# Optimization experiments

Measured on AMD Instinct MI355X. Metric: run time of the kernel, lower is better.

Reference implementation:

```python
import jax, jax.numpy as jnp
import numpy as np
from jax import lax

EPS_LN = 1e-5
EPS_BN = 1e-5

def layernorm(x, g, b):
    m = x.mean(-1, keepdims=True)
    v = x.var(-1, keepdims=True)
    return (x - m) / jnp.sqrt(v + EPS_LN) * g + b

def conv(x, w, b):
    y = lax.conv_general_dilated(x, w, (1, 1), 'SAME', dimension_numbers=('NCHW', 'OIHW', 'NCHW'))
    return y + b[None, :, None, None]

def bnorm(x, g, b, m, v):
    # BatchNorm2d in eval mode (running stats)
    return (x - m[None, :, None, None]) / jnp.sqrt(v[None, :, None, None] + EPS_BN) * g[None, :, None, None] + b[None, :, None, None]

def maxpool2(x):
    return lax.reduce_window(x, -jnp.inf, lax.max, (1, 1, 2, 2), (1, 1, 2, 2), 'VALID')

def l2norm_rows(x):
    n = jnp.linalg.norm(x, axis=1, keepdims=True)
    return x / jnp.maximum(n, 1e-12)

def fastslow(x, sw, sb, fw, fb, lng, lnb, lr, decay):
    # one hebbian fast-weight update step (torch does this in no_grad on x.detach())
    xs = lax.stop_gradient(x)
    fw = fw * decay
    fb = fb * decay
    slow_out = xs @ sw.T + sb
    xn = l2norm_rows(xs)
    son = l2norm_rows(slow_out)
    hebb = son.T @ xn / xs.shape[0]          # [out,in] outer-product update
    fw = fw + lr * hebb
    wn = jnp.linalg.norm(fw, axis=1, keepdims=True)
    fw = jnp.where(wn > 0.25, fw * (0.25 / (wn + 1e-8)), fw)
    fb = jnp.clip(fb + lr * son.mean(0), -0.2, 0.2)
    fw = lax.stop_gradient(fw)
    fb = lax.stop_gradient(fb)
    out = x @ (sw + fw).T + (sb + fb)
    return layernorm(out, lng, lnb)

def forward(x, c1_w, c1_b, bn1_g, bn1_b, bn1_m, bn1_v,
            c2_w, c2_b, bn2_g, bn2_b, bn2_m, bn2_v,
            c3_w, c3_b, bn3_g, bn3_b, bn3_m, bn3_v,
            core_w, core_b, core_lng, core_lnb,
            fp_sw, fp_sb, fp_fw, fp_fb, fp_lng, fp_lnb,
            sp_sw, sp_sb, sp_fw, sp_fb, sp_lng, sp_lnb,
            int_w, int_b, int_lng, int_lnb, mem,
            cn_w1, cn_b1, cn_lng, cn_lnb, cn_w2, cn_b2,
            pr_w, pr_b, pr_lng, pr_lnb, cl_w, cl_b):
    # encoder (dropout layers are identity in eval)
    h = jax.nn.relu(bnorm(conv(x, c1_w, c1_b), bn1_g, bn1_b, bn1_m, bn1_v)); h = maxpool2(h)
    h = jax.nn.relu(bnorm(conv(h, c2_w, c2_b), bn2_g, bn2_b, bn2_m, bn2_v)); h = maxpool2(h)
    h = jax.nn.relu(bnorm(conv(h, c3_w, c3_b), bn3_g, bn3_b, bn3_m, bn3_v))
    h = h.mean((2, 3))  # AdaptiveAvgPool2d((1,1)) + Flatten -> [B,256]
    # core
    hc = jax.nn.relu(layernorm(h @ core_w.T + core_b, core_lng, core_lnb))
    # dual system: memory EMA (no_grad), fast/slow hebbian paths, integrator
    mem_new = lax.stop_gradient(0.9 * mem + 0.1 * hc.mean(0, keepdims=True))
    fast_out = fastslow(hc, fp_sw, fp_sb, fp_fw, fp_fb, fp_lng, fp_lnb, 0.015, 0.95)
    slow_out = fastslow(hc + 0.3 * mem_new, sp_sw, sp_sb, sp_fw, sp_fb, sp_lng, sp_lnb, 0.005, 0.97)
    comb = jnp.concatenate([fast_out, slow_out], axis=1)
    hd = layernorm(comb @ int_w.T + int_b, int_lng, int_lnb)
    hd = hd + hc  # residual
    # consciousness: phi from eigen-entropy of feature covariance (no_grad)
    a = lax.stop_gradient(hd)
    am = a.mean(0, keepdims=True)
    ast = jnp.std(a, axis=0, keepdims=True, ddof=1) + 1e-6
    an = (a - am) / ast
    n = a.shape[0]
    cov = an.T @ an / (n - 1) + 1e-4 * jnp.eye(a.shape[1], dtype=a.dtype)
    eigs = jnp.clip(jnp.linalg.eigvalsh(cov), 0.0, None)
    en = eigs / (eigs.sum() + 1e-8)
    entropy = -(en * jnp.log(en + 1e-8)).sum()
    phi = entropy / jnp.log(jnp.asarray(float(a.shape[1]), a.dtype))
    phi_eff = jnp.clip(0.3 * phi, 0.0, 1.0)  # running_phi starts at 0: 0.7*0 + 0.3*phi
    net = jax.nn.relu(layernorm(hd @ cn_w1.T + cn_b1, cn_lng, cn_lnb)) @ cn_w2.T + cn_b2
    strength = jax.nn.sigmoid((phi_eff - 0.1) * 5.0)
    coef = jnp.where(phi_eff > 0.1, strength, 0.1)
    hcon = hd + coef * net
    # projection + classifier
    hp = jax.nn.relu(layernorm(hcon @ pr_w.T + pr_b, pr_lng, pr_lnb))
    return hp @ cl_w.T + cl_b

def setup_inputs() -> dict:
    key = jax.random.key(0)
    ks = iter(jax.random.split(key, 64))
    def nrm(shape, s=0.05):
        return jax.random.normal(next(ks), shape, jnp.float32) * s
    B, D = 512, 256
    d = {}
    d['x'] = jax.random.normal(next(ks), (B, 3, 32, 32), jnp.float32)
    for i, (co, ci) in enumerate([(64, 3), (128, 64), (256, 128)], 1):
        d[f'c{i}_w'] = nrm((co, ci, 3, 3))
        d[f'c{i}_b'] = jnp.zeros((co,), jnp.float32)
        d[f'bn{i}_g'] = jnp.ones((co,), jnp.float32)
        d[f'bn{i}_b'] = jnp.zeros((co,), jnp.float32)
        d[f'bn{i}_m'] = jnp.zeros((co,), jnp.float32)
        d[f'bn{i}_v'] = jnp.ones((co,), jnp.float32)
    d['core_w'] = nrm((D, D)); d['core_b'] = jnp.zeros((D,), jnp.float32)
    d['core_lng'] = jnp.ones((D,), jnp.float32); d['core_lnb'] = jnp.zeros((D,), jnp.float32)
    for p in ['fp', 'sp']:
        d[f'{p}_sw'] = nrm((D, D)); d[f'{p}_sb'] = jnp.zeros((D,), jnp.float32)
        d[f'{p}_fw'] = nrm((D, D), 0.01); d[f'{p}_fb'] = jnp.zeros((D,), jnp.float32)
        d[f'{p}_lng'] = jnp.ones((D,), jnp.float32); d[f'{p}_lnb'] = jnp.zeros((D,), jnp.float32)
    d['int_w'] = nrm((D, 2 * D)); d['int_b'] = jnp.zeros((D,), jnp.float32)
    d['int_lng'] = jnp.ones((D,), jnp.float32); d['int_lnb'] = jnp.zeros((D,), jnp.float32)
    d['mem'] = jnp.zeros((1, D), jnp.float32)
    d['cn_w1'] = nrm((D, D)); d['cn_b1'] = jnp.zeros((D,), jnp.float32)
    d['cn_lng'] = jnp.ones((D,), jnp.float32); d['cn_lnb'] = jnp.zeros((D,), jnp.float32)
    d['cn_w2'] = nrm((D, D)); d['cn_b2'] = jnp.zeros((D,), jnp.float32)
    d['pr_w'] = nrm((128, D)); d['pr_b'] = jnp.zeros((128,), jnp.float32)
    d['pr_lng'] = jnp.ones((128,), jnp.float32); d['pr_lnb'] = jnp.zeros((128,), jnp.float32)
    d['cl_w'] = nrm((10, 128)); d['cl_b'] = jnp.zeros((10,), jnp.float32)
    return d

def reference(x, c1_w, c1_b, bn1_g, bn1_b, bn1_m, bn1_v,
              c2_w, c2_b, bn2_g, bn2_b, bn2_m, bn2_v,
              c3_w, c3_b, bn3_g, bn3_b, bn3_m, bn3_v,
              core_w, core_b, core_lng, core_lnb,
              fp_sw, fp_sb, fp_fw, fp_fb, fp_lng, fp_lnb,
              sp_sw, sp_sb, sp_fw, sp_fb, sp_lng, sp_lnb,
              int_w, int_b, int_lng, int_lnb, mem,
              cn_w1, cn_b1, cn_lng, cn_lnb, cn_w2, cn_b2,
              pr_w, pr_b, pr_lng, pr_lnb, cl_w, cl_b):
    return forward(x, c1_w, c1_b, bn1_g, bn1_b, bn1_m, bn1_v,
                   c2_w, c2_b, bn2_g, bn2_b, bn2_m, bn2_v,
                   c3_w, c3_b, bn3_g, bn3_b, bn3_m, bn3_v,
                   core_w, core_b, core_lng, core_lnb,
                   fp_sw, fp_sb, fp_fw, fp_fb, fp_lng, fp_lnb,
                   sp_sw, sp_sb, sp_fw, sp_fb, sp_lng, sp_lnb,
                   int_w, int_b, int_lng, int_lnb, mem,
                   cn_w1, cn_b1, cn_lng, cn_lnb, cn_w2, cn_b2,
                   pr_w, pr_b, pr_lng, pr_lnb, cl_w, cl_b)
```

## Files before the change

kernel.cpp:

```cpp
#include <hip/hip_runtime.h>
#include <hip/hip_bf16.h>

template<int NT>
__device__ __forceinline__ float block_sum(float v, float* red, int t) {
  red[t] = v; __syncthreads();
#pragma unroll
  for (int s = NT/2; s > 0; s >>= 1) {
    if (t < s) red[t] += red[t+s];
    __syncthreads();
  }
  float r = red[0];
  __syncthreads();
  return r;
}

template<int DIN>
__device__ __forceinline__ float dot_f32_row(const float* __restrict__ wr, const float* __restrict__ xs) {
  float acc = 0.f;
  const float4* wp = reinterpret_cast<const float4*>(wr);
#pragma unroll 4
  for (int i = 0; i < DIN/4; ++i) {
    float4 w4 = wp[i];
    acc += w4.x*xs[i*4] + w4.y*xs[i*4+1] + w4.z*xs[i*4+2] + w4.w*xs[i*4+3];
  }
  return acc;
}

__global__ __launch_bounds__(256) void k_conv1(const float* __restrict__ x, const float* __restrict__ w1,
    const float* __restrict__ cb, const float* __restrict__ g, const float* __restrict__ bb,
    const float* __restrict__ m, const float* __restrict__ v, float* __restrict__ p1)
{
  __shared__ float xs[3][34][34];
  __shared__ float ws1[64*27];
  __shared__ float A1[64], B1[64];
  int b = blockIdx.x, t = threadIdx.x;
  float* xsf = &xs[0][0][0];
  for (int i = t; i < 3*34*34; i += 256) xsf[i] = 0.f;
  for (int i = t; i < 64*27; i += 256) ws1[i] = w1[i];
  if (t < 64) {
    float sc = g[t] * rsqrtf(v[t] + 1e-5f);
    A1[t] = sc;
    B1[t] = (cb[t] - m[t])*sc + bb[t];
  }
  __syncthreads();
  for (int i = t; i < 3*1024; i += 256) {
    int ci = i >> 10, rem = i & 1023, y = rem >> 5, xx = rem & 31;
    xs[ci][y+1][xx+1] = x[((size_t)b*3 + ci)*1024 + rem];
  }
  __syncthreads();
  int py = t >> 4, px = t & 15;
  int y0 = py*2, x0 = px*2;
  for (int co = 0; co < 64; ++co) {
    float a00=0.f,a01=0.f,a10=0.f,a11=0.f;
#pragma unroll
    for (int ci = 0; ci < 3; ++ci) {
      const float* xb = &xs[ci][y0][x0];
      float r0a=xb[0],r0b=xb[1],r0c=xb[2],r0d=xb[3];
      float r1a=xb[34],r1b=xb[35],r1c=xb[36],r1d=xb[37];
      float r2a=xb[68],r2b=xb[69],r2c=xb[70],r2d=xb[71];
      float r3a=xb[102],r3b=xb[103],r3c=xb[104],r3d=xb[105];
      const float* wp = &ws1[co*27 + ci*9];
      float ww0=wp[0],ww1=wp[1],ww2=wp[2],ww3=wp[3],ww4=wp[4],ww5=wp[5],ww6=wp[6],ww7=wp[7],ww8=wp[8];
      a00 += ww0*r0a+ww1*r0b+ww2*r0c + ww3*r1a+ww4*r1b+ww5*r1c + ww6*r2a+ww7*r2b+ww8*r2c;
      a01 += ww0*r0b+ww1*r0c+ww2*r0d + ww3*r1b+ww4*r1c+ww5*r1d + ww6*r2b+ww7*r2c+ww8*r2d;
      a10 += ww0*r1a+ww1*r1b+ww2*r1c + ww3*r2a+ww4*r2b+ww5*r2c + ww6*r3a+ww7*r3b+ww8*r3c;
      a11 += ww0*r1b+ww1*r1c+ww2*r1d + ww3*r2b+ww4*r2c+ww5*r2d + ww6*r3b+ww7*r3c+ww8*r3d;
    }
    float sc = A1[co], sh = B1[co];
    float vmax = fmaxf(fmaxf(a00*sc+sh, a01*sc+sh), fmaxf(a10*sc+sh, a11*sc+sh));
    vmax = fmaxf(vmax, 0.f);
    p1[(((size_t)b*64 + co)*16 + py)*16 + px] = vmax;
  }
}

__global__ __launch_bounds__(256) void k_conv2(const float* __restrict__ p1, const float* __restrict__ w2,
    const float* __restrict__ cb, const float* __restrict__ g, const float* __restrict__ bb,
    const float* __restrict__ m, const float* __restrict__ v, float* __restrict__ p2)
{
  __shared__ float xs[64][18][18];
  __shared__ float wchT[576*5];
  __shared__ float A2[128], B2[128];
  int b = blockIdx.x, t = threadIdx.x;
  float* xsf = &xs[0][0][0];
  for (int i = t; i < 64*18*18; i += 256) xsf[i] = 0.f;
  if (t < 128) {
    float sc = g[t] * rsqrtf(v[t] + 1e-5f);
    A2[t] = sc;
    B2[t] = (cb[t] - m[t])*sc + bb[t];
  }
  __syncthreads();
  for (int i = t; i < 64*256; i += 256) {
    int ci = i >> 8, rem = i & 255, y = rem >> 4, xx = rem & 15;
    xs[ci][y+1][xx+1] = p1[((size_t)b*64 + ci)*256 + rem];
  }
  int lane = t & 3, pos = t >> 2;
  int py = pos >> 3, px = pos & 7;
  int y0 = py*2, x0 = px*2;
  for (int it = 0; it < 32; ++it) {
    __syncthreads();
    for (int i = t; i < 2304; i += 256) {
      int rem = i % 576, co = i / 576;
      wchT[rem*5 + co] = w2[(size_t)it*2304 + i];
    }
    __syncthreads();
    float a00=0.f,a01=0.f,a10=0.f,a11=0.f;
    for (int ci = 0; ci < 64; ++ci) {
      const float* xb = &xs[ci][y0][x0];
      float r0a=xb[0],r0b=xb[1],r0c=xb[2],r0d=xb[3];
      float r1a=xb[18],r1b=xb[19],r1c=xb[20],r1d=xb[21];
      float r2a=xb[36],r2b=xb[37],r2c=xb[38],r2d=xb[39];
      float r3a=xb[54],r3b=xb[55],r3c=xb[56],r3d=xb[57];
      const float* wp = &wchT[(ci*9)*5 + lane];
      float ww0=wp[0],ww1=wp[5],ww2=wp[10],ww3=wp[15],ww4=wp[20],ww5=wp[25],ww6=wp[30],ww7=wp[35],ww8=wp[40];
      a00 += ww0*r0a+ww1*r0b+ww2*r0c + ww3*r1a+ww4*r1b+ww5*r1c + ww6*r2a+ww7*r2b+ww8*r2c;
      a01 += ww0*r0b+ww1*r0c+ww2*r0d + ww3*r1b+ww4*r1c+ww5*r1d + ww6*r2b+ww7*r2c+ww8*r2d;
      a10 += ww0*r1a+ww1*r1b+ww2*r1c + ww3*r2a+ww4*r2b+ww5*r2c + ww6*r3a+ww7*r3b+ww8*r3c;
      a11 += ww0*r1b+ww1*r1c+ww2*r1d + ww3*r2b+ww4*r2c+ww5*r2d + ww6*r3b+ww7*r3c+ww8*r3d;
    }
    int co = it*4 + lane;
    float sc = A2[co], sh = B2[co];
    float vmax = fmaxf(fmaxf(a00*sc+sh, a01*sc+sh), fmaxf(a10*sc+sh, a11*sc+sh));
    vmax = fmaxf(vmax, 0.f);
    p2[(((size_t)b*128 + co)*8 + py)*8 + px] = vmax;
  }
}

__global__ __launch_bounds__(256) void k_conv3(const float* __restrict__ p2, const float* __restrict__ w3,
    const float* __restrict__ cb, const float* __restrict__ g, const float* __restrict__ bb,
    const float* __restrict__ m, const float* __restrict__ v, float* __restrict__ h)
{
  __shared__ float xs[128][10][10];
  __shared__ float wchT[1152*17];
  __shared__ float A3[256], B3[256];
  __shared__ float red2[256];
  int b = blockIdx.x, t = threadIdx.x;
  float* xsf = &xs[0][0][0];
  for (int i = t; i < 128*100; i += 256) xsf[i] = 0.f;
  {
    float sc = g[t] * rsqrtf(v[t] + 1e-5f);
    A3[t] = sc;
    B3[t] = (cb[t] - m[t])*sc + bb[t];
  }
  __syncthreads();
  for (int i = t; i < 128*64; i += 256) {
    int ci = i >> 6, rem = i & 63, y = rem >> 3, xx = rem & 7;
    xs[ci][y+1][xx+1] = p2[((size_t)b*128 + ci)*64 + rem];
  }
  int lane = t & 15, cluster = t >> 4;
  int cy = cluster >> 2, cx = cluster & 3;
  int y0 = cy*2, x0 = cx*2;
  for (int it = 0; it < 16; ++it) {
    __syncthreads();
    for (int i = t; i < 18432; i += 256) {
      int rem = i % 1152, co = i / 1152;
      wchT[rem*17 + co] = w3[(size_t)it*18432 + i];
    }
    __syncthreads();
    float a00=0.f,a01=0.f,a10=0.f,a11=0.f;
    for (int ci = 0; ci < 128; ++ci) {
      const float* xb = &xs[ci][y0][x0];
      float r0a=xb[0],r0b=xb[1],r0c=xb[2],r0d=xb[3];
      float r1a=xb[10],r1b=xb[11],r1c=xb[12],r1d=xb[13];
      float r2a=xb[20],r2b=xb[21],r2c=xb[22],r2d=xb[23];
      float r3a=xb[30],r3b=xb[31],r3c=xb[32],r3d=xb[33];
      const float* wp = &wchT[(ci*9)*17 + lane];
      float ww0=wp[0],ww1=wp[17],ww2=wp[34],ww3=wp[51],ww4=wp[68],ww5=wp[85],ww6=wp[102],ww7=wp[119],ww8=wp[136];
      a00 += ww0*r0a+ww1*r0b+ww2*r0c + ww3*r1a+ww4*r1b+ww5*r1c + ww6*r2a+ww7*r2b+ww8*r2c;
      a01 += ww0*r0b+ww1*r0c+ww2*r0d + ww3*r1b+ww4*r1c+ww5*r1d + ww6*r2b+ww7*r2c+ww8*r2d;
      a10 += ww0*r1a+ww1*r1b+ww2*r1c + ww3*r2a+ww4*r2b+ww5*r2c + ww6*r3a+ww7*r3b+ww8*r3c;
      a11 += ww0*r1b+ww1*r1c+ww2*r1d + ww3*r2b+ww4*r2c+ww5*r2d + ww6*r3b+ww7*r3c+ww8*r3d;
    }
    int co = it*16 + lane;
    float sc = A3[co], sh = B3[co];
    float local = fmaxf(a00*sc+sh,0.f)+fmaxf(a01*sc+sh,0.f)+fmaxf(a10*sc+sh,0.f)+fmaxf(a11*sc+sh,0.f);
    red2[cluster*16 + lane] = local;
    __syncthreads();
    if (t < 16) {
      float s2 = 0.f;
      for (int c2 = 0; c2 < 16; ++c2) s2 += red2[c2*16 + t];
      h[(size_t)b*256 + it*16 + t] = s2 * (1.f/64.f);
    }
  }
}

template<int DIN, int DOUT, bool RELU, bool RESID>
__global__ __launch_bounds__(DOUT) void k_lin_ln(
    const float* __restrict__ in, const float* __restrict__ W, const float* __restrict__ bias,
    const float* __restrict__ g, const float* __restrict__ be,
    const float* __restrict__ resid, float* __restrict__ out, int ostride, int ooff)
{
  __shared__ float xs[DIN];
  __shared__ float red[DOUT];
  int b = blockIdx.x, t = threadIdx.x;
  for (int i = t; i < DIN; i += DOUT) xs[i] = in[(size_t)b*DIN + i];
  __syncthreads();
  float acc = dot_f32_row<DIN>(W + (size_t)t*DIN, xs) + bias[t];
  float mean = block_sum<DOUT>(acc, red, t) * (1.f/DOUT);
  float dv = acc - mean;
  float var = block_sum<DOUT>(dv*dv, red, t) * (1.f/DOUT);
  float y = dv * rsqrtf(var + 1e-5f) * g[t] + be[t];
  if (RELU) y = fmaxf(y, 0.f);
  if (RESID) y += resid[(size_t)b*DOUT + t];
  out[(size_t)b*ostride + ooff + t] = y;
}

__global__ __launch_bounds__(256) void k_lin_rownorm(const float* __restrict__ in, const float* __restrict__ sw,
    const float* __restrict__ sb, float* __restrict__ sout, float* __restrict__ xninv, float* __restrict__ sninv)
{
  int b = blockIdx.x, t = threadIdx.x;
  __shared__ float xs[256];
  __shared__ float red[256];
  xs[t] = in[(size_t)b*256 + t];
  __syncthreads();
  float acc = dot_f32_row<256>(sw + (size_t)t*256, xs) + sb[t];
  sout[(size_t)b*256 + t] = acc;
  float xn2 = block_sum<256>(xs[t]*xs[t], red, t);
  float sn2 = block_sum<256>(acc*acc, red, t);
  if (t == 0) {
    xninv[b] = 1.f / fmaxf(sqrtf(xn2), 1e-12f);
    sninv[b] = 1.f / fmaxf(sqrtf(sn2), 1e-12f);
  }
}

__global__ __launch_bounds__(256) void k_hebb(const float* __restrict__ x, const float* __restrict__ s,
    const float* __restrict__ xninv, const float* __restrict__ sninv,
    const float* __restrict__ sw, const float* __restrict__ fw,
    const float* __restrict__ sb, const float* __restrict__ fb,
    float lr, float decay, float* __restrict__ weff, float* __restrict__ beff)
{
  int o = blockIdx.x, t = threadIdx.x;
  __shared__ float c[512];
  __shared__ float sonb[512];
  __shared__ float red[256];
  for (int b = t; b < 512; b += 256) {
    float son = s[(size_t)b*256 + o] * sninv[b];
    sonb[b] = son;
    c[b] = son * xninv[b];
  }
  __syncthreads();
  float acc = 0.f;
  for (int b = 0; b < 512; ++b) acc += c[b] * x[(size_t)b*256 + t];
  float hebb = acc * (1.f/512.f);
  float fwn = fw[(size_t)o*256 + t] * decay + lr * hebb;
  float wn2 = block_sum<256>(fwn*fwn, red, t);
  float wn = sqrtf(wn2);
  float scale = (wn > 0.25f) ? 0.25f/(wn + 1e-8f) : 1.f;
  weff[(size_t)o*256 + t] = sw[(size_t)o*256 + t] + fwn*scale;
  float sm = block_sum<256>(sonb[t] + sonb[t+256], red, t) * (1.f/512.f);
  if (t == 0) {
    float fbe = fb[o] * decay + lr * sm;
    fbe = fminf(fmaxf(fbe, -0.2f), 0.2f);
    beff[o] = sb[o] + fbe;
  }
}

__global__ __launch_bounds__(256) void k_mem(const float* __restrict__ hc, const float* __restrict__ mem,
                                             float* __restrict__ memnew)
{
  int t = threadIdx.x;
  float s = 0.f;
  for (int b = 0; b < 512; ++b) s += hc[(size_t)b*256 + t];
  memnew[t] = 0.9f*mem[t] + 0.1f*(s * (1.f/512.f));
}

__global__ __launch_bounds__(256) void k_x2(const float* __restrict__ hc, const float* __restrict__ memnew,
                                            float* __restrict__ x2)
{
  int i = blockIdx.x*256 + threadIdx.x;
  x2[i] = hc[i] + 0.3f*memnew[i & 255];
}

__global__ __launch_bounds__(256) void k_colstats(const float* __restrict__ hd, float* __restrict__ am,
                                                  float* __restrict__ ainv)
{
  int t = threadIdx.x;
  float s1 = 0.f;
  for (int b = 0; b < 512; ++b) s1 += hd[(size_t)b*256 + t];
  float mean = s1 * (1.f/512.f);
  float s2 = 0.f;
  for (int b = 0; b < 512; ++b) { float dv = hd[(size_t)b*256 + t] - mean; s2 += dv*dv; }
  am[t] = mean;
  ainv[t] = 1.f/(sqrtf(s2 * (1.f/511.f)) + 1e-6f);
}

__global__ __launch_bounds__(256) void k_cov(const float* __restrict__ hd, const float* __restrict__ am,
    const float* __restrict__ ainv, float* __restrict__ cov)
{
  int i = blockIdx.x, t = threadIdx.x;
  __shared__ float ci[512];
  float ami = am[i], aii = ainv[i];
  for (int b = t; b < 512; b += 256) ci[b] = (hd[(size_t)b*256 + i] - ami)*aii;
  __syncthreads();
  float amj = am[t], aij = ainv[t];
  float acc = 0.f;
  for (int b = 0; b < 512; ++b) acc += ci[b] * (hd[(size_t)b*256 + t] - amj);
  float cval = acc * aij * (1.f/511.f) + ((i == t) ? 1e-4f : 0.f);
  cov[(size_t)i*256 + t] = cval;
}

__global__ __launch_bounds__(256) void k_tridiag(float* __restrict__ A, float* __restrict__ d, float* __restrict__ e)
{
  const int n = 256;
  int t = threadIdx.x;
  __shared__ float v[256], q[256], red[256];
  __shared__ float sH, salpha;
  for (int k = 0; k < n-2; ++k) {
    int m = n-1-k;
    int base = k+1;
    float xi = (t < m) ? A[(size_t)k*n + base + t] : 0.f;
    float sigma = block_sum<256>(xi*xi, red, t);
    if (t == 0) {
      float x0 = A[(size_t)base*n + k];
      float alpha = (x0 >= 0.f) ? -sqrtf(sigma) : sqrtf(sigma);
      salpha = alpha;
      sH = sigma - x0*alpha;
      e[k] = alpha;
    }
    __syncthreads();
    float H = sH;
    if (H <= 1e-32f) { __syncthreads(); continue; }
    if (t < m) v[t] = (t == 0) ? (xi - salpha) : xi;
    __syncthreads();
    float pt = 0.f;
    if (t < m) {
      const float* col = A + (size_t)base*n + (base + t);
      int j = 0;
      for (; j + 16 <= m; j += 16) {
        const float* cj = col + (size_t)j*n;
        float a0=cj[0],      a1=cj[256],    a2=cj[512],    a3=cj[768];
        float a4=cj[1024],   a5=cj[1280],   a6=cj[1536],   a7=cj[1792];
        float a8=cj[2048],   a9=cj[2304],   a10=cj[2560],  a11=cj[2816];
        float a12=cj[3072],  a13=cj[3328],  a14=cj[3584],  a15=cj[3840];
        pt += a0*v[j]    + a1*v[j+1]  + a2*v[j+2]  + a3*v[j+3]
            + a4*v[j+4]  + a5*v[j+5]  + a6*v[j+6]  + a7*v[j+7]
            + a8*v[j+8]  + a9*v[j+9]  + a10*v[j+10]+ a11*v[j+11]
            + a12*v[j+12]+ a13*v[j+13]+ a14*v[j+14]+ a15*v[j+15];
      }
      for (; j < m; ++j) pt += col[(size_t)j*n] * v[j];
      pt /= H;
    }
    float Kv = block_sum<256>((t < m) ? v[t]*pt : 0.f, red, t) / (2.f*H);
    if (t < m) q[t] = pt - Kv*v[t];
    __syncthreads();
    if (t < m) {
      float vt = v[t], qt = q[t];
      float* col = A + (size_t)base*n + (base + t);
      int j = 0;
      for (; j + 8 <= m; j += 8) {
        float* cj = col + (size_t)j*n;
        float a0=cj[0],    a1=cj[256],  a2=cj[512],  a3=cj[768];
        float a4=cj[1024], a5=cj[1280], a6=cj[1536], a7=cj[1792];
        float b0 = v[j]*qt   + q[j]*vt;
        float b1 = v[j+1]*qt + q[j+1]*vt;
        float b2 = v[j+2]*qt + q[j+2]*vt;
        float b3 = v[j+3]*qt + q[j+3]*vt;
        float b4 = v[j+4]*qt + q[j+4]*vt;
        float b5 = v[j+5]*qt + q[j+5]*vt;
        float b6 = v[j+6]*qt + q[j+6]*vt;
        float b7 = v[j+7]*qt + q[j+7]*vt;
        cj[0]=a0-b0; cj[256]=a1-b1; cj[512]=a2-b2; cj[768]=a3-b3;
        cj[1024]=a4-b4; cj[1280]=a5-b5; cj[1536]=a6-b6; cj[1792]=a7-b7;
      }
      for (; j < m; ++j) col[(size_t)j*n] -= v[j]*qt + q[j]*vt;
    }
    __syncthreads();
  }
  if (t == 0) { e[n-2] = A[(size_t)(n-1)*n + (n-2)]; e[n-1] = 0.f; }
  if (t < n) d[t] = A[(size_t)t*n + t];
}

__global__ __launch_bounds__(256) void k_eig_coef(const float* __restrict__ dg, const float* __restrict__ eg,
                                                  float* __restrict__ coefout)
{
  const int n = 256;
  int t = threadIdx.x;
  __shared__ float sd[256], se2[256], sea[256], red[256];
  sd[t] = dg[t];
  float ev = (t < n-1) ? eg[t] : 0.f;
  se2[t] = ev*ev;
  sea[t] = fabsf(ev);
  __syncthreads();
  float r = ((t > 0) ? sea[t-1] : 0.f) + sea[t];
  red[t] = sd[t] - r; __syncthreads();
  for (int s = 128; s > 0; s >>= 1) { if (t < s) red[t] = fminf(red[t], red[t+s]); __syncthreads(); }
  float glo = red[0] - 1e-3f; __syncthreads();
  red[t] = sd[t] + r; __syncthreads();
  for (int s = 128; s > 0; s >>= 1) { if (t < s) red[t] = fmaxf(red[t], red[t+s]); __syncthreads(); }
  float ghi = red[0] + 1e-3f; __syncthreads();

  float lo = glo, hi = ghi;
  for (int it = 0; it < 40; ++it) {
    float mid = 0.5f*(lo + hi);
    int cnt = 0;
    float qq = sd[0] - mid;
    cnt += (qq < 0.f);
    for (int i = 1; i < n; ++i) {
      float denom = qq;
      if (fabsf(denom) < 1e-20f) denom = (denom < 0.f) ? -1e-20f : 1e-20f;
      qq = sd[i] - mid - se2[i-1]/denom;
      cnt += (qq < 0.f);
    }
    if (cnt <= t) lo = mid; else hi = mid;
  }
  float lam = fmaxf(0.5f*(lo + hi), 0.f);
  float tot = block_sum<256>(lam, red, t) + 1e-8f;
  float en = lam / tot;
  float contrib = -en * logf(en + 1e-8f);
  float ent = block_sum<256>(contrib, red, t);
  if (t == 0) {
    float phi = ent / logf(256.f);
    float phi_eff = fminf(fmaxf(0.3f*phi, 0.f), 1.f);
    float strength = 1.f/(1.f + expf(-(phi_eff - 0.1f)*5.f));
    coefout[0] = (phi_eff > 0.1f) ? strength : 0.1f;
  }
}

__global__ __launch_bounds__(256) void k_cn2(const float* __restrict__ t1, const float* __restrict__ W,
    const float* __restrict__ bias, const float* __restrict__ hd, const float* __restrict__ coefp,
    float* __restrict__ hcon)
{
  __shared__ float xs[256];
  int b = blockIdx.x, t = threadIdx.x;
  xs[t] = t1[(size_t)b*256 + t];
  __syncthreads();
  float acc = dot_f32_row<256>(W + (size_t)t*256, xs) + bias[t];
  hcon[(size_t)b*256 + t] = hd[(size_t)b*256 + t] + coefp[0]*acc;
}

__global__ __launch_bounds__(64) void k_cls(const float* __restrict__ hp, const float* __restrict__ W,
    const float* __restrict__ bias, float* __restrict__ out)
{
  int b = blockIdx.x, t = threadIdx.x;
  __shared__ float xs[128];
  if (t < 64) { xs[t] = hp[(size_t)b*128 + t]; xs[t+64] = hp[(size_t)b*128 + t + 64]; }
  __syncthreads();
  if (t < 10) {
    float acc = bias[t];
    const float* wr = W + (size_t)t*128;
    for (int i = 0; i < 128; ++i) acc += wr[i]*xs[i];
    out[(size_t)b*10 + t] = acc;
  }
}

extern "C" void kernel_launch(void* const* d_in, const int* in_sizes, int n_in,
                              void* d_out, int out_size, void* d_ws, size_t ws_size,
                              hipStream_t stream)
{
  (void)in_sizes; (void)n_in; (void)out_size; (void)ws_size;
  const float* x     = (const float*)d_in[0];
  const float* c1w   = (const float*)d_in[1];
  const float* c1b   = (const float*)d_in[2];
  const float* bn1g  = (const float*)d_in[3];
  const float* bn1b  = (const float*)d_in[4];
  const float* bn1m  = (const float*)d_in[5];
  const float* bn1v  = (const float*)d_in[6];
  const float* c2w   = (const float*)d_in[7];
  const float* c2b   = (const float*)d_in[8];
  const float* bn2g  = (const float*)d_in[9];
  const float* bn2b  = (const float*)d_in[10];
  const float* bn2m  = (const float*)d_in[11];
  const float* bn2v  = (const float*)d_in[12];
  const float* c3w   = (const float*)d_in[13];
  const float* c3b   = (const float*)d_in[14];
  const float* bn3g  = (const float*)d_in[15];
  const float* bn3b  = (const float*)d_in[16];
  const float* bn3m  = (const float*)d_in[17];
  const float* bn3v  = (const float*)d_in[18];
  const float* corew = (const float*)d_in[19];
  const float* coreb = (const float*)d_in[20];
  const float* corelng = (const float*)d_in[21];
  const float* corelnb = (const float*)d_in[22];
  const float* fpsw  = (const float*)d_in[23];
  const float* fpsb  = (const float*)d_in[24];
  const float* fpfw  = (const float*)d_in[25];
  const float* fpfb  = (const float*)d_in[26];
  const float* fplng = (const float*)d_in[27];
  const float* fplnb = (const float*)d_in[28];
  const float* spsw  = (const float*)d_in[29];
  const float* spsb  = (const float*)d_in[30];
  const float* spfw  = (const float*)d_in[31];
  const float* spfb  = (const float*)d_in[32];
  const float* splng = (const float*)d_in[33];
  const float* splnb = (const float*)d_in[34];
  const float* intw  = (const float*)d_in[35];
  const float* intb  = (const float*)d_in[36];
  const float* intlng= (const float*)d_in[37];
  const float* intlnb= (const float*)d_in[38];
  const float* memi  = (const float*)d_in[39];
  const float* cnw1  = (const float*)d_in[40];
  const float* cnb1  = (const float*)d_in[41];
  const float* cnlng = (const float*)d_in[42];
  const float* cnlnb = (const float*)d_in[43];
  const float* cnw2  = (const float*)d_in[44];
  const float* cnb2  = (const float*)d_in[45];
  const float* prw   = (const float*)d_in[46];
  const float* prb   = (const float*)d_in[47];
  const float* prlng = (const float*)d_in[48];
  const float* prlnb = (const float*)d_in[49];
  const float* clw   = (const float*)d_in[50];
  const float* clb   = (const float*)d_in[51];
  float* out = (float*)d_out;

  float* w = (float*)d_ws;
  size_t off = 0;
  auto alloc = [&](size_t nel) { float* p = w + off; off += nel; return p; };
  float* p1     = alloc((size_t)512*64*16*16);
  float* p2     = alloc((size_t)512*128*8*8);
  float* h      = alloc(512*256);
  float* hc     = alloc(512*256);
  float* x2     = alloc(512*256);
  float* s      = alloc(512*256);
  float* xninv  = alloc(512);
  float* sninv  = alloc(512);
  float* memnew = alloc(256);
  float* weff   = alloc(256*256);
  float* beff   = alloc(256);
  float* comb   = alloc((size_t)512*512);
  float* hd     = alloc(512*256);
  float* am     = alloc(256);
  float* ainv   = alloc(256);
  float* cov    = alloc(256*256);
  float* dvec   = alloc(256);
  float* evec   = alloc(256);
  float* coefb  = alloc(8);
  float* t1     = alloc(512*256);
  float* hcon   = alloc(512*256);
  float* hp     = alloc(512*128);

  k_conv1<<<512,256,0,stream>>>(x, c1w, c1b, bn1g, bn1b, bn1m, bn1v, p1);
  k_conv2<<<512,256,0,stream>>>(p1, c2w, c2b, bn2g, bn2b, bn2m, bn2v, p2);
  k_conv3<<<512,256,0,stream>>>(p2, c3w, c3b, bn3g, bn3b, bn3m, bn3v, h);
  k_lin_ln<256,256,true,false><<<512,256,0,stream>>>(h, corew, coreb, corelng, corelnb, nullptr, hc, 256, 0);
  k_mem<<<1,256,0,stream>>>(hc, memi, memnew);
  k_x2<<<512,256,0,stream>>>(hc, memnew, x2);
  k_lin_rownorm<<<512,256,0,stream>>>(hc, fpsw, fpsb, s, xninv, sninv);
  k_hebb<<<256,256,0,stream>>>(hc, s, xninv, sninv, fpsw, fpfw, fpsb, fpfb, 0.015f, 0.95f, weff, beff);
  k_lin_ln<256,256,false,false><<<512,256,0,stream>>>(hc, weff, beff, fplng, fplnb, nullptr, comb, 512, 0);
  k_lin_rownorm<<<512,256,0,stream>>>(x2, spsw, spsb, s, xninv, sninv);
  k_hebb<<<256,256,0,stream>>>(x2, s, xninv, sninv, spsw, spfw, spsb, spfb, 0.005f, 0.97f, weff, beff);
  k_lin_ln<256,256,false,false><<<512,256,0,stream>>>(x2, weff, beff, splng, splnb, nullptr, comb, 512, 256);
  k_lin_ln<512,256,false,true><<<512,256,0,stream>>>(comb, intw, intb, intlng, intlnb, hc, hd, 256, 0);
  k_colstats<<<1,256,0,stream>>>(hd, am, ainv);
  k_cov<<<256,256,0,stream>>>(hd, am, ainv, cov);
  k_tridiag<<<1,256,0,stream>>>(cov, dvec, evec);
  k_eig_coef<<<1,256,0,stream>>>(dvec, evec, coefb);
  k_lin_ln<256,256,true,false><<<512,256,0,stream>>>(hd, cnw1, cnb1, cnlng, cnlnb, nullptr, t1, 256, 0);
  k_cn2<<<512,256,0,stream>>>(t1, cnw2, cnb2, hd, coefb, hcon);
  k_lin_ln<256,128,true,false><<<512,128,0,stream>>>(hcon, prw, prb, prlng, prlnb, nullptr, hp, 128, 0);
  k_cls<<<512,64,0,stream>>>(hp, clw, clb, out);
}
```

Before: 4.565 ms.

## Keep tridiagonalization matrix as packed lower triangle in shared memory

The Householder tridiagonalization kernel now copies the lower triangle of the symmetric matrix into a packed LDS array and does all matvec and rank-2 updates there instead of in global memory. Only the lower triangle is updated, which halves the update work. Block reductions switch from a shared-memory tree to wavefront shuffles. This uses about 128KB of LDS and has irregular packed indexing that may cause bank conflicts and thread imbalance.

After: 4.820 ms. 5.6% more time.

```diff
diff --git a/kernel.cpp b/kernel.cpp
--- a/kernel.cpp
+++ b/kernel.cpp
@@ -10,6 +10,16 @@
     __syncthreads();
   }
   float r = red[0];
+  __syncthreads();
+  return r;
+}
+
+__device__ __forceinline__ float block_sum4(float val, float* red4, int t) {
+#pragma unroll
+  for (int mk = 1; mk < 64; mk <<= 1) val += __shfl_xor(val, mk, 64);
+  if ((t & 63) == 0) red4[t >> 6] = val;
+  __syncthreads();
+  float r = red4[0] + red4[1] + red4[2] + red4[3];
   __syncthreads();
   return r;
 }
@@ -298,19 +308,33 @@
   cov[(size_t)i*256 + t] = cval;
 }
 
-__global__ __launch_bounds__(256) void k_tridiag(float* __restrict__ A, float* __restrict__ d, float* __restrict__ e)
+__global__ __launch_bounds__(256) void k_tridiag(const float* __restrict__ A, float* __restrict__ d, float* __restrict__ e)
 {
   const int n = 256;
+  __shared__ float tri[32896];
+  __shared__ float v[256], q[256];
+  __shared__ float red4[4];
+  __shared__ float sH, salpha;
   int t = threadIdx.x;
-  __shared__ float v[256], q[256], red[256];
-  __shared__ float sH, salpha;
+
+  for (int i = t; i < 32896; i += 256) {
+    int r = (int)((sqrtf(8.f*(float)i + 1.f) - 1.f) * 0.5f);
+    while ((r+1)*(r+2)/2 <= i) ++r;
+    while (r*(r+1)/2 > i) --r;
+    int c = i - r*(r+1)/2;
+    tri[i] = A[(size_t)r*n + c];
+  }
+  __syncthreads();
+
   for (int k = 0; k < n-2; ++k) {
     int m = n-1-k;
     int base = k+1;
-    float xi = (t < m) ? A[(size_t)k*n + base + t] : 0.f;
-    float sigma = block_sum<256>(xi*xi, red, t);
+    int R = base + t;
+    int offA = (R*(R+1))/2 + base;
+    float xi = (t < m) ? tri[offA - 1] : 0.f;
+    float sigma = block_sum4(xi*xi, red4, t);
     if (t == 0) {
-      float x0 = A[(size_t)base*n + k];
+      float x0 = tri[(base*(base+1))/2 + k];
       float alpha = (x0 >= 0.f) ? -sqrtf(sigma) : sqrtf(sigma);
       salpha = alpha;
       sH = sigma - x0*alpha;
@@ -321,52 +345,63 @@
     if (H <= 1e-32f) { __syncthreads(); continue; }
     if (t < m) v[t] = (t == 0) ? (xi - salpha) : xi;
     __syncthreads();
+
     float pt = 0.f;
     if (t < m) {
-      const float* col = A + (size_t)base*n + (base + t);
+      float a0 = 0.f, a1 = 0.f, a2 = 0.f, a3 = 0.f;
       int j = 0;
-      for (; j + 16 <= m; j += 16) {
-        const float* cj = col + (size_t)j*n;
-        float a0=cj[0],      a1=cj[256],    a2=cj[512],    a3=cj[768];
-        float a4=cj[1024],   a5=cj[1280],   a6=cj[1536],   a7=cj[1792];
-        float a8=cj[2048],   a9=cj[2304],   a10=cj[2560],  a11=cj[2816];
-        float a12=cj[3072],  a13=cj[3328],  a14=cj[3584],  a15=cj[3840];
-        pt += a0*v[j]    + a1*v[j+1]  + a2*v[j+2]  + a3*v[j+3]
-            + a4*v[j+4]  + a5*v[j+5]  + a6*v[j+6]  + a7*v[j+7]
-            + a8*v[j+8]  + a9*v[j+9]  + a10*v[j+10]+ a11*v[j+11]
-            + a12*v[j+12]+ a13*v[j+13]+ a14*v[j+14]+ a15*v[j+15];
+      for (; j + 4 <= t+1; j += 4) {
+        a0 += tri[offA + j]     * v[j];
+        a1 += tri[offA + j + 1] * v[j+1];
+        a2 += tri[offA + j + 2] * v[j+2];
+        a3 += tri[offA + j + 3] * v[j+3];
       }
-      for (; j < m; ++j) pt += col[(size_t)j*n] * v[j];
-      pt /= H;
-    }
-    float Kv = block_sum<256>((t < m) ? v[t]*pt : 0.f, red, t) / (2.f*H);
+      for (; j <= t; ++j) a0 += tri[offA + j] * v[j];
+      int Rj = R + 1;
+      int off = (Rj*(Rj+1))/2 + R;
+      for (j = t+1; j + 4 <= m; j += 4) {
+        int o0 = off;
+        int o1 = o0 + (base + j + 1);
+        int o2 = o1 + (base + j + 2);
+        int o3 = o2 + (base + j + 3);
+        a0 += tri[o0] * v[j];
+        a1 += tri[o1] * v[j+1];
+        a2 += tri[o2] * v[j+2];
+        a3 += tri[o3] * v[j+3];
+        off = o3 + (base + j + 4);
+      }
+      for (; j < m; ++j) {
+        a0 += tri[off] * v[j];
+        off += (base + j + 1);
+      }
+      pt = (a0 + a1 + a2 + a3) / H;
+    }
+    float Kv = block_sum4((t < m) ? v[t]*pt : 0.f, red4, t) / (2.f*H);
     if (t < m) q[t] = pt - Kv*v[t];
     __syncthreads();
+
     if (t < m) {
       float vt = v[t], qt = q[t];
-      float* col = A + (size_t)base*n + (base + t);
-      int j = 0;
-      for (; j + 8 <= m; j += 8) {
-        float* cj = col + (size_t)j*n;
-        float a0=cj[0],    a1=cj[256],  a2=cj[512],  a3=cj[768];
-        float a4=cj[1024], a5=cj[1280], a6=cj[1536], a7=cj[1792];
-        float b0 = v[j]*qt   + q[j]*vt;
-        float b1 = v[j+1]*qt + q[j+1]*vt;
-        float b2 = v[j+2]*qt + q[j+2]*vt;
-        float b3 = v[j+3]*qt + q[j+3]*vt;
-        float b4 = v[j+4]*qt + q[j+4]*vt;
-        float b5 = v[j+5]*qt + q[j+5]*vt;
-        float b6 = v[j+6]*qt + q[j+6]*vt;
-        float b7 = v[j+7]*qt + q[j+7]*vt;
-        cj[0]=a0-b0; cj[256]=a1-b1; cj[512]=a2-b2; cj[768]=a3-b3;
-        cj[1024]=a4-b4; cj[1280]=a5-b5; cj[1536]=a6-b6; cj[1792]=a7-b7;
+      int c = 0;
+      for (; c + 4 <= t+1; c += 4) {
+        float u0 = tri[offA + c]     - (vt*q[c]   + qt*v[c]);
+        float u1 = tri[offA + c + 1] - (vt*q[c+1] + qt*v[c+1]);
+        float u2 = tri[offA + c + 2] - (vt*q[c+2] + qt*v[c+2]);
+        float u3 = tri[offA + c + 3] - (vt*q[c+3] + qt*v[c+3]);
+        tri[offA + c]     = u0;
+        tri[offA + c + 1] = u1;
+        tri[offA + c + 2] = u2;
+        tri[offA + c + 3] = u3;
       }
-      for (; j < m; ++j) col[(size_t)j*n] -= v[j]*qt + q[j]*vt;
-    }
-    __syncthreads();
-  }
-  if (t == 0) { e[n-2] = A[(size_t)(n-1)*n + (n-2)]; e[n-1] = 0.f; }
-  if (t < n) d[t] = A[(size_t)t*n + t];
+      for (; c <= t; ++c) tri[offA + c] -= vt*q[c] + qt*v[c];
+    }
+    __syncthreads();
+  }
+  if (t == 0) {
+    e[n-2] = tri[((n-1)*n)/2 + (n-2)];
+    e[n-1] = 0.f;
+  }
+  d[t] = tri[(t*(t+1))/2 + t];
 }
 
 __global__ __launch_bounds__(256) void k_eig_coef(const float* __restrict__ dg, const float* __restrict__ eg,
```
